# Kernel optimization log

Measured on AMD Instinct MI355X. Metric: run time of the kernel, lower is better.

The kernel has to match this reference:

```python
import jax, jax.numpy as jnp
import numpy as np

MARGIN = 0.3
N = 8192
D = 256
NUM_CLASSES = 64


def setup_inputs() -> dict:
    key = jax.random.key(0)
    k1, k2 = jax.random.split(key)
    embeddings = jax.random.normal(k1, (N, D), dtype=jnp.float32)
    labels = jax.random.randint(k2, (N,), 0, NUM_CLASSES, dtype=jnp.int64)
    return {"embeddings": embeddings, "labels": labels}


def _pairwise_euclidean(x):
    # torch.cdist(x, x, p=2): sqrt of squared distances, safe at 0
    sq = jnp.sum(x * x, axis=-1)                       # [N]
    d2 = sq[:, None] + sq[None, :] - 2.0 * (x @ x.T)   # [N, N]
    d2 = jnp.maximum(d2, 0.0)
    pos = d2 > 0
    return jnp.where(pos, jnp.sqrt(jnp.where(pos, d2, 1.0)), 0.0)


def reference(embeddings, labels):
    d = _pairwise_euclidean(embeddings)                # [N, N]
    same = labels[:, None] == labels[None, :]          # [N, N] pos_mask (incl. self)
    neg = ~same                                        # neg_mask
    pos_nz = same & (d > 0.0)                          # pos_dist[pos_dist > 0]

    hardest_pos = jnp.max(jnp.where(pos_nz, d, -jnp.inf), axis=1)  # [N]
    hardest_neg = jnp.min(jnp.where(neg, d, jnp.inf), axis=1)      # [N]

    # valid anchors: >1 positives (incl. self), >=1 negative, and a nonzero pos dist
    valid = (jnp.sum(same, axis=1) > 1) & jnp.any(neg, axis=1) & jnp.any(pos_nz, axis=1)

    per_anchor = jnp.where(valid,
                           jax.nn.relu(hardest_pos - hardest_neg + MARGIN),
                           0.0)
    count = jnp.sum(valid.astype(jnp.float32))
    return jnp.where(count > 0,
                     jnp.sum(per_anchor) / jnp.maximum(count, 1.0),
                     0.0)
```

## Files before the change

### kernel.cpp

```cpp
#include <hip/hip_runtime.h>


#define N_PTS 8192
#define DIM   256
#define MARGIN 0.3f

typedef __attribute__((ext_vector_type(8))) short bf16x8;
typedef __attribute__((ext_vector_type(4))) float f32x4;

__device__ __forceinline__ unsigned short f2bf(float f) {
    unsigned u = __float_as_uint(f);
    u += 0x7FFFu + ((u >> 16) & 1u);
    return (unsigned short)(u >> 16);
}

__global__ void prep_kernel(const float* __restrict__ X,
                            unsigned short* __restrict__ Xb,
                            float* __restrict__ sq) {
    int t = blockIdx.x * 256 + threadIdx.x;
    {
        int row = t >> 6, lane = t & 63;
        float4 v = reinterpret_cast<const float4*>(X)[t];
        float p = v.x * v.x + v.y * v.y + v.z * v.z + v.w * v.w;
        #pragma unroll
        for (int m = 1; m < 64; m <<= 1) p += __shfl_xor(p, m, 64);
        if (lane == 0) sq[row] = p;
    }
    {
        int i    = t & 1023;
        int Rg   = t >> 10;
        int half = i & 1;
        int lsub = (i >> 1) & 15;
        int lgrp = (i >> 5) & 3;
        int kk   = (i >> 7) & 7;
        int row  = Rg * 16 + lsub;
        int sidx = row * 64 + kk * 8 + lgrp * 2 + half;
        float4 v = reinterpret_cast<const float4*>(X)[sidx];
        ushort4 b4;
        b4.x = f2bf(v.x); b4.y = f2bf(v.y); b4.z = f2bf(v.z); b4.w = f2bf(v.w);
        reinterpret_cast<ushort4*>(Xb)[t] = b4;
    }
}

__launch_bounds__(512, 2)
__global__ void mine_kernel(const unsigned short* __restrict__ Xb,
                            const float* __restrict__ sq,
                            const int* __restrict__ labels,
                            float* __restrict__ vp,
                            float* __restrict__ vn) {
    int bid = blockIdx.x;
    int panel = bid >> 2;
    int q     = bid & 3;
    int tid = threadIdx.x;
    int w = tid >> 6, l = tid & 63;
    int wr = w >> 2, wc = w & 3;
    int lsub = l & 15, lgrp = l >> 4;

    const float INF = __int_as_float(0x7f800000);

    const unsigned short* abase = Xb + (size_t)(panel * 8 + wr * 4) * 4096 + l * 8;
    bf16x8 a[4][8];
    #pragma unroll
    for (int m = 0; m < 4; ++m)
        #pragma unroll
        for (int kk = 0; kk < 8; ++kk)
            a[m][kk] = *reinterpret_cast<const bf16x8*>(abase + m * 4096 + kk * 512);

    int rowbase = panel * 128 + wr * 64;
    int lrj[4][4];
    #pragma unroll
    for (int m = 0; m < 4; ++m)
        #pragma unroll
        for (int j = 0; j < 4; ++j)
            lrj[m][j] = labels[rowbase + m * 16 + lgrp * 4 + j];

    float vpr[4][4], vnr[4][4];
    #pragma unroll
    for (int m = 0; m < 4; ++m)
        #pragma unroll
        for (int j = 0; j < 4; ++j) { vpr[m][j] = -INF; vnr[m][j] = INF; }

    int colwave = q * 2048 + wc * 512;
    const unsigned short* bbase = Xb + (size_t)(colwave >> 4) * 4096 + l * 8;

    for (int cs = 0; cs < 16; ++cs) {
        int colbase = colwave + cs * 32;
        int lc0 = labels[colbase + lsub];
        int lc1 = labels[colbase + 16 + lsub];
        float sc0 = sq[colbase + lsub];
        float sc1 = sq[colbase + 16 + lsub];

        f32x4 acc[4][2];
        #pragma unroll
        for (int m = 0; m < 4; ++m) {
            acc[m][0] = (f32x4){0.f, 0.f, 0.f, 0.f};
            acc[m][1] = (f32x4){0.f, 0.f, 0.f, 0.f};
        }

        const unsigned short* bb = bbase + (size_t)cs * 8192;
        #pragma unroll
        for (int kp = 0; kp < 4; ++kp) {
            bf16x8 b00 = *reinterpret_cast<const bf16x8*>(bb + kp * 1024);
            bf16x8 b01 = *reinterpret_cast<const bf16x8*>(bb + 4096 + kp * 1024);
            bf16x8 b10 = *reinterpret_cast<const bf16x8*>(bb + kp * 1024 + 512);
            bf16x8 b11 = *reinterpret_cast<const bf16x8*>(bb + 4096 + kp * 1024 + 512);
            #pragma unroll
            for (int m = 0; m < 4; ++m) {
                acc[m][0] = __builtin_amdgcn_mfma_f32_16x16x32_bf16(
                    a[m][2 * kp], b00, acc[m][0], 0, 0, 0);
                acc[m][1] = __builtin_amdgcn_mfma_f32_16x16x32_bf16(
                    a[m][2 * kp], b01, acc[m][1], 0, 0, 0);
            }
            #pragma unroll
            for (int m = 0; m < 4; ++m) {
                acc[m][0] = __builtin_amdgcn_mfma_f32_16x16x32_bf16(
                    a[m][2 * kp + 1], b10, acc[m][0], 0, 0, 0);
                acc[m][1] = __builtin_amdgcn_mfma_f32_16x16x32_bf16(
                    a[m][2 * kp + 1], b11, acc[m][1], 0, 0, 0);
            }
        }

        #pragma unroll
        for (int m = 0; m < 4; ++m)
            #pragma unroll
            for (int j = 0; j < 4; ++j) {
                int lr = lrj[m][j];
                float v0 = fmaf(-2.f, acc[m][0][j], sc0);
                float v1 = fmaf(-2.f, acc[m][1][j], sc1);
                bool s0 = (lr == lc0), s1 = (lr == lc1);
                vpr[m][j] = fmaxf(vpr[m][j], s0 ? v0 : -INF);
                vpr[m][j] = fmaxf(vpr[m][j], s1 ? v1 : -INF);
                vnr[m][j] = fminf(vnr[m][j], s0 ? INF : v0);
                vnr[m][j] = fminf(vnr[m][j], s1 ? INF : v1);
            }
    }

    int slot = q * 4 + wc;
    #pragma unroll
    for (int m = 0; m < 4; ++m)
        #pragma unroll
        for (int j = 0; j < 4; ++j) {
            float p = vpr[m][j], n = vnr[m][j];
            #pragma unroll
            for (int s = 1; s < 16; s <<= 1) {
                p = fmaxf(p, __shfl_xor(p, s, 64));
                n = fminf(n, __shfl_xor(n, s, 64));
            }
            if (lsub == 0) {
                int row = rowbase + m * 16 + lgrp * 4 + j;
                vp[slot * N_PTS + row] = p;
                vn[slot * N_PTS + row] = n;
            }
        }
}

__global__ void finalizeA_kernel(const float* __restrict__ vp,
                                 const float* __restrict__ vn,
                                 const float* __restrict__ sq,
                                 const int* __restrict__ labels,
                                 float* __restrict__ bsum,
                                 float* __restrict__ bcnt) {
    __shared__ int hist[64];
    __shared__ float ss[4], cc[4];
    int tid = threadIdx.x;
    if (tid < 64) hist[tid] = 0;
    __syncthreads();
    for (int i = tid; i < N_PTS; i += 256) atomicAdd(&hist[labels[i]], 1);
    __syncthreads();

    const float INF = __int_as_float(0x7f800000);
    int r = blockIdx.x * 256 + tid;
    float mp = -INF, mn = INF;
    #pragma unroll
    for (int s = 0; s < 16; ++s) {
        mp = fmaxf(mp, vp[s * N_PTS + r]);
        mn = fminf(mn, vn[s * N_PTS + r]);
    }
    float sr = sq[r];
    float hp2 = sr + mp;
    float hn2 = fmaxf(sr + mn, 0.f);
    int h = hist[labels[r]];
    bool valid = (h > 1) && (h < N_PTS) && (hp2 > 0.f);
    float contrib = valid ? fmaxf(sqrtf(hp2) - sqrtf(hn2) + MARGIN, 0.f) : 0.f;
    float cnt = valid ? 1.f : 0.f;

    #pragma unroll
    for (int m = 1; m < 64; m <<= 1) {
        contrib += __shfl_xor(contrib, m, 64);
        cnt     += __shfl_xor(cnt, m, 64);
    }
    int wv = tid >> 6, lv = tid & 63;
    if (lv == 0) { ss[wv] = contrib; cc[wv] = cnt; }
    __syncthreads();
    if (tid == 0) {
        bsum[blockIdx.x] = ss[0] + ss[1] + ss[2] + ss[3];
        bcnt[blockIdx.x] = cc[0] + cc[1] + cc[2] + cc[3];
    }
}

__global__ void finalizeB_kernel(const float* __restrict__ bsum,
                                 const float* __restrict__ bcnt,
                                 float* __restrict__ out) {
    int l = threadIdx.x;
    float s = (l < 32) ? bsum[l] : 0.f;
    float c = (l < 32) ? bcnt[l] : 0.f;
    #pragma unroll
    for (int m = 1; m < 64; m <<= 1) {
        s += __shfl_xor(s, m, 64);
        c += __shfl_xor(c, m, 64);
    }
    if (l == 0) out[0] = (c > 0.f) ? (s / c) : 0.f;
}

extern "C" void kernel_launch(void* const* d_in, const int* in_sizes, int n_in,
                              void* d_out, int out_size, void* d_ws, size_t ws_size,
                              hipStream_t stream) {
    const float* X      = (const float*)d_in[0];
    const int*   labels = (const int*)d_in[1];
    float*       out    = (float*)d_out;

    char* ws = (char*)d_ws;
    unsigned short* Xb = (unsigned short*)ws;
    float* sq   = (float*)(ws + 4194304);
    float* vp   = (float*)(ws + 4194304 + 32768);
    float* vn   = (float*)(ws + 4194304 + 32768 + 524288);
    float* bsum = (float*)(ws + 4194304 + 32768 + 1048576);
    float* bcnt = (float*)(ws + 4194304 + 32768 + 1048576 + 128);

    prep_kernel<<<2048, 256, 0, stream>>>(X, Xb, sq);
    mine_kernel<<<256, 512, 0, stream>>>(Xb, sq, labels, vp, vn);
    finalizeA_kernel<<<32, 256, 0, stream>>>(vp, vn, sq, labels, bsum, bcnt);
    finalizeB_kernel<<<1, 64, 0, stream>>>(bsum, bcnt, out);
}
```

Baseline: 112.9 us.

## Restructure mining kernel with LDS-staged row bands, register-resident columns, fused finalize

The mining kernel now holds a 64-column B tile in registers per wave and streams 512-row bands through double-buffered, XOR-swizzled LDS using global_load_lds, with a swizzled block order. It writes per-column partial max/min, relying on the symmetry of the distance matrix. The prep kernel drops the fragment-layout repack in favour of plain row-major bf16, and the two finalize kernels merge into one that uses atomics and a last-block counter. The aim is better reuse and fewer launches, at the cost of LDS traffic, barriers, and atomic ordering risk.

```diff
diff --git a/kernel.cpp b/kernel.cpp
--- a/kernel.cpp
+++ b/kernel.cpp
@@ -14,32 +14,23 @@
     return (unsigned short)(u >> 16);
 }
 
-__global__ void prep_kernel(const float* __restrict__ X,
-                            unsigned short* __restrict__ Xb,
-                            float* __restrict__ sq) {
+__global__ __launch_bounds__(256)
+void prep_kernel(const float* __restrict__ X,
+                 unsigned short* __restrict__ Xb,
+                 float* __restrict__ sq,
+                 float* __restrict__ gsum) {
     int t = blockIdx.x * 256 + threadIdx.x;
-    {
-        int row = t >> 6, lane = t & 63;
-        float4 v = reinterpret_cast<const float4*>(X)[t];
-        float p = v.x * v.x + v.y * v.y + v.z * v.z + v.w * v.w;
-        #pragma unroll
-        for (int m = 1; m < 64; m <<= 1) p += __shfl_xor(p, m, 64);
-        if (lane == 0) sq[row] = p;
-    }
-    {
-        int i    = t & 1023;
-        int Rg   = t >> 10;
-        int half = i & 1;
-        int lsub = (i >> 1) & 15;
-        int lgrp = (i >> 5) & 3;
-        int kk   = (i >> 7) & 7;
-        int row  = Rg * 16 + lsub;
-        int sidx = row * 64 + kk * 8 + lgrp * 2 + half;
-        float4 v = reinterpret_cast<const float4*>(X)[sidx];
-        ushort4 b4;
-        b4.x = f2bf(v.x); b4.y = f2bf(v.y); b4.z = f2bf(v.z); b4.w = f2bf(v.w);
-        reinterpret_cast<ushort4*>(Xb)[t] = b4;
-    }
+    int row = t >> 6, lane = t & 63;
+    float4 v = reinterpret_cast<const float4*>(X)[t];
+    ushort4 b4;
+    b4.x = f2bf(v.x); b4.y = f2bf(v.y); b4.z = f2bf(v.z); b4.w = f2bf(v.w);
+    reinterpret_cast<ushort4*>(Xb)[t] = b4;
+    float p = v.x * v.x + v.y * v.y + v.z * v.z + v.w * v.w;
+    #pragma unroll
+    for (int m = 1; m < 64; m <<= 1) p += __shfl_xor(p, m, 64);
+    if (lane == 0) sq[row] = p;
+    if (blockIdx.x == 0 && threadIdx.x < 3)
+        gsum[threadIdx.x] = 0.f;
 }
 
 __launch_bounds__(512, 2)
@@ -48,118 +39,138 @@
                             const int* __restrict__ labels,
                             float* __restrict__ vp,
                             float* __restrict__ vn) {
+    __shared__ unsigned short buf[2][64 * 256];
+
     int bid = blockIdx.x;
-    int panel = bid >> 2;
-    int q     = bid & 3;
+    int swz = (bid & 7) * 32 + (bid >> 3);
+    int cg = swz >> 4;
+    int rb = swz & 15;
+
     int tid = threadIdx.x;
     int w = tid >> 6, l = tid & 63;
-    int wr = w >> 2, wc = w & 3;
     int lsub = l & 15, lgrp = l >> 4;
+    int C0 = cg * 512 + w * 64;
 
     const float INF = __int_as_float(0x7f800000);
 
-    const unsigned short* abase = Xb + (size_t)(panel * 8 + wr * 4) * 4096 + l * 8;
-    bf16x8 a[4][8];
-    #pragma unroll
-    for (int m = 0; m < 4; ++m)
-        #pragma unroll
-        for (int kk = 0; kk < 8; ++kk)
-            a[m][kk] = *reinterpret_cast<const bf16x8*>(abase + m * 4096 + kk * 512);
-
-    int rowbase = panel * 128 + wr * 64;
-    int lrj[4][4];
-    #pragma unroll
-    for (int m = 0; m < 4; ++m)
-        #pragma unroll
-        for (int j = 0; j < 4; ++j)
-            lrj[m][j] = labels[rowbase + m * 16 + lgrp * 4 + j];
-
-    float vpr[4][4], vnr[4][4];
-    #pragma unroll
-    for (int m = 0; m < 4; ++m)
-        #pragma unroll
-        for (int j = 0; j < 4; ++j) { vpr[m][j] = -INF; vnr[m][j] = INF; }
-
-    int colwave = q * 2048 + wc * 512;
-    const unsigned short* bbase = Xb + (size_t)(colwave >> 4) * 4096 + l * 8;
-
-    for (int cs = 0; cs < 16; ++cs) {
-        int colbase = colwave + cs * 32;
-        int lc0 = labels[colbase + lsub];
-        int lc1 = labels[colbase + 16 + lsub];
-        float sc0 = sq[colbase + lsub];
-        float sc1 = sq[colbase + 16 + lsub];
-
-        f32x4 acc[4][2];
-        #pragma unroll
-        for (int m = 0; m < 4; ++m) {
-            acc[m][0] = (f32x4){0.f, 0.f, 0.f, 0.f};
-            acc[m][1] = (f32x4){0.f, 0.f, 0.f, 0.f};
-        }
-
-        const unsigned short* bb = bbase + (size_t)cs * 8192;
-        #pragma unroll
-        for (int kp = 0; kp < 4; ++kp) {
-            bf16x8 b00 = *reinterpret_cast<const bf16x8*>(bb + kp * 1024);
-            bf16x8 b01 = *reinterpret_cast<const bf16x8*>(bb + 4096 + kp * 1024);
-            bf16x8 b10 = *reinterpret_cast<const bf16x8*>(bb + kp * 1024 + 512);
-            bf16x8 b11 = *reinterpret_cast<const bf16x8*>(bb + 4096 + kp * 1024 + 512);
+    bf16x8 b[4][8];
+    {
+        const unsigned short* pb = Xb + (size_t)(C0 + lsub) * DIM + lgrp * 8;
+        #pragma unroll
+        for (int n = 0; n < 4; ++n)
+            #pragma unroll
+            for (int kk = 0; kk < 8; ++kk)
+                b[n][kk] = *reinterpret_cast<const bf16x8*>(
+                    pb + (size_t)n * 16 * DIM + kk * 32);
+    }
+    int lc4[4];
+    #pragma unroll
+    for (int n = 0; n < 4; ++n) lc4[n] = labels[C0 + n * 16 + lsub];
+
+    float hpc[4], hnc[4];
+    #pragma unroll
+    for (int n = 0; n < 4; ++n) { hpc[n] = -INF; hnc[n] = INF; }
+
+    int band = rb * 512;
+    int xorv = lsub & 7;
+
+    {
+        const unsigned short* src = Xb + (size_t)band * DIM;
+        #pragma unroll
+        for (int i = 0; i < 4; ++i) {
+            int p = i * 512 + tid;
+            int row = p >> 5, slot = p & 31;
+            int kc = slot ^ (row & 7);
+            __builtin_amdgcn_global_load_lds(
+                (const __attribute__((address_space(1))) void*)(src + row * DIM + kc * 8),
+                (__attribute__((address_space(3))) void*)(&buf[0][p * 8]),
+                16, 0, 0);
+        }
+    }
+    __syncthreads();
+
+    int cur = 0;
+    for (int c = 0; c < 8; ++c) {
+        if (c < 7) {
+            const unsigned short* src = Xb + (size_t)(band + (c + 1) * 64) * DIM;
+            #pragma unroll
+            for (int i = 0; i < 4; ++i) {
+                int p = i * 512 + tid;
+                int row = p >> 5, slot = p & 31;
+                int kc = slot ^ (row & 7);
+                __builtin_amdgcn_global_load_lds(
+                    (const __attribute__((address_space(1))) void*)(src + row * DIM + kc * 8),
+                    (__attribute__((address_space(3))) void*)(&buf[cur ^ 1][p * 8]),
+                    16, 0, 0);
+            }
+        }
+
+        const unsigned short* bc = buf[cur];
+        f32x4 acc[4][4];
+        #pragma unroll
+        for (int m = 0; m < 4; ++m)
+            #pragma unroll
+            for (int n = 0; n < 4; ++n) acc[m][n] = (f32x4){0.f, 0.f, 0.f, 0.f};
+
+        #pragma unroll
+        for (int kk = 0; kk < 8; ++kk) {
+            bf16x8 a[4];
             #pragma unroll
             for (int m = 0; m < 4; ++m) {
-                acc[m][0] = __builtin_amdgcn_mfma_f32_16x16x32_bf16(
-                    a[m][2 * kp], b00, acc[m][0], 0, 0, 0);
-                acc[m][1] = __builtin_amdgcn_mfma_f32_16x16x32_bf16(
-                    a[m][2 * kp], b01, acc[m][1], 0, 0, 0);
+                int rowA = m * 16 + lsub;
+                int slot = (kk * 4 + lgrp) ^ xorv;
+                a[m] = *reinterpret_cast<const bf16x8*>(&bc[rowA * 256 + slot * 8]);
             }
             #pragma unroll
-            for (int m = 0; m < 4; ++m) {
-                acc[m][0] = __builtin_amdgcn_mfma_f32_16x16x32_bf16(
-                    a[m][2 * kp + 1], b10, acc[m][0], 0, 0, 0);
-                acc[m][1] = __builtin_amdgcn_mfma_f32_16x16x32_bf16(
-                    a[m][2 * kp + 1], b11, acc[m][1], 0, 0, 0);
+            for (int m = 0; m < 4; ++m)
+                #pragma unroll
+                for (int n = 0; n < 4; ++n)
+                    acc[m][n] = __builtin_amdgcn_mfma_f32_16x16x32_bf16(
+                        a[m], b[n][kk], acc[m][n], 0, 0, 0);
+        }
+
+        int rowg = band + c * 64 + lgrp * 4;
+        #pragma unroll
+        for (int m = 0; m < 4; ++m)
+            #pragma unroll
+            for (int j = 0; j < 4; ++j) {
+                int gr = rowg + m * 16 + j;
+                int lr = labels[gr];
+                float sr = sq[gr];
+                #pragma unroll
+                for (int n = 0; n < 4; ++n) {
+                    float v = fmaf(-2.f, acc[m][n][j], sr);
+                    bool same = (lr == lc4[n]);
+                    hpc[n] = same ? fmaxf(hpc[n], v) : hpc[n];
+                    hnc[n] = same ? hnc[n] : fminf(hnc[n], v);
+                }
             }
-        }
-
-        #pragma unroll
-        for (int m = 0; m < 4; ++m)
-            #pragma unroll
-            for (int j = 0; j < 4; ++j) {
-                int lr = lrj[m][j];
-                float v0 = fmaf(-2.f, acc[m][0][j], sc0);
-                float v1 = fmaf(-2.f, acc[m][1][j], sc1);
-                bool s0 = (lr == lc0), s1 = (lr == lc1);
-                vpr[m][j] = fmaxf(vpr[m][j], s0 ? v0 : -INF);
-                vpr[m][j] = fmaxf(vpr[m][j], s1 ? v1 : -INF);
-                vnr[m][j] = fminf(vnr[m][j], s0 ? INF : v0);
-                vnr[m][j] = fminf(vnr[m][j], s1 ? INF : v1);
-            }
-    }
-
-    int slot = q * 4 + wc;
-    #pragma unroll
-    for (int m = 0; m < 4; ++m)
-        #pragma unroll
-        for (int j = 0; j < 4; ++j) {
-            float p = vpr[m][j], n = vnr[m][j];
-            #pragma unroll
-            for (int s = 1; s < 16; s <<= 1) {
-                p = fmaxf(p, __shfl_xor(p, s, 64));
-                n = fminf(n, __shfl_xor(n, s, 64));
-            }
-            if (lsub == 0) {
-                int row = rowbase + m * 16 + lgrp * 4 + j;
-                vp[slot * N_PTS + row] = p;
-                vn[slot * N_PTS + row] = n;
-            }
-        }
-}
-
-__global__ void finalizeA_kernel(const float* __restrict__ vp,
-                                 const float* __restrict__ vn,
-                                 const float* __restrict__ sq,
-                                 const int* __restrict__ labels,
-                                 float* __restrict__ bsum,
-                                 float* __restrict__ bcnt) {
+
+        if (c < 7) __syncthreads();
+        cur ^= 1;
+    }
+
+    #pragma unroll
+    for (int n = 0; n < 4; ++n) {
+        float p = hpc[n], q = hnc[n];
+        p = fmaxf(p, __shfl_xor(p, 16, 64));
+        q = fminf(q, __shfl_xor(q, 16, 64));
+        p = fmaxf(p, __shfl_xor(p, 32, 64));
+        q = fminf(q, __shfl_xor(q, 32, 64));
+        if (l < 16) {
+            int col = C0 + n * 16 + l;
+            vp[rb * N_PTS + col] = p;
+            vn[rb * N_PTS + col] = q;
+        }
+    }
+}
+
+__global__ void finalize_kernel(const float* __restrict__ vp,
+                                const float* __restrict__ vn,
+                                const float* __restrict__ sq,
+                                const int* __restrict__ labels,
+                                float* __restrict__ gsum,
+                                float* __restrict__ out) {
     __shared__ int hist[64];
     __shared__ float ss[4], cc[4];
     int tid = threadIdx.x;
@@ -169,18 +180,18 @@
     __syncthreads();
 
     const float INF = __int_as_float(0x7f800000);
-    int r = blockIdx.x * 256 + tid;
+    int c = blockIdx.x * 256 + tid;
     float mp = -INF, mn = INF;
     #pragma unroll
     for (int s = 0; s < 16; ++s) {
-        mp = fmaxf(mp, vp[s * N_PTS + r]);
-        mn = fminf(mn, vn[s * N_PTS + r]);
-    }
-    float sr = sq[r];
-    float hp2 = sr + mp;
-    float hn2 = fmaxf(sr + mn, 0.f);
-    int h = hist[labels[r]];
-    bool valid = (h > 1) && (h < N_PTS) && (hp2 > 0.f);
+        mp = fmaxf(mp, vp[s * N_PTS + c]);
+        mn = fminf(mn, vn[s * N_PTS + c]);
+    }
+    float sc = sq[c];
+    float hp2 = sc + mp;
+    float hn2 = fmaxf(sc + mn, 0.f);
+    int h = hist[labels[c]];
+    bool valid = (h > 1) && (hp2 > 0.f);
     float contrib = valid ? fmaxf(sqrtf(hp2) - sqrtf(hn2) + MARGIN, 0.f) : 0.f;
     float cnt = valid ? 1.f : 0.f;
 
@@ -193,23 +204,16 @@
     if (lv == 0) { ss[wv] = contrib; cc[wv] = cnt; }
     __syncthreads();
     if (tid == 0) {
-        bsum[blockIdx.x] = ss[0] + ss[1] + ss[2] + ss[3];
-        bcnt[blockIdx.x] = cc[0] + cc[1] + cc[2] + cc[3];
-    }
-}
-
-__global__ void finalizeB_kernel(const float* __restrict__ bsum,
-                                 const float* __restrict__ bcnt,
-                                 float* __restrict__ out) {
-    int l = threadIdx.x;
-    float s = (l < 32) ? bsum[l] : 0.f;
-    float c = (l < 32) ? bcnt[l] : 0.f;
-    #pragma unroll
-    for (int m = 1; m < 64; m <<= 1) {
-        s += __shfl_xor(s, m, 64);
-        c += __shfl_xor(c, m, 64);
-    }
-    if (l == 0) out[0] = (c > 0.f) ? (s / c) : 0.f;
+        atomicAdd(&gsum[0], ss[0] + ss[1] + ss[2] + ss[3]);
+        atomicAdd(&gsum[1], cc[0] + cc[1] + cc[2] + cc[3]);
+        __threadfence();
+        unsigned old = atomicAdd(reinterpret_cast<unsigned*>(&gsum[2]), 1u);
+        if (old == 31u) {
+            float S = atomicAdd(&gsum[0], 0.f);
+            float C = atomicAdd(&gsum[1], 0.f);
+            out[0] = (C > 0.f) ? (S / C) : 0.f;
+        }
+    }
 }
 
 extern "C" void kernel_launch(void* const* d_in, const int* in_sizes, int n_in,
@@ -224,11 +228,9 @@
     float* sq   = (float*)(ws + 4194304);
     float* vp   = (float*)(ws + 4194304 + 32768);
     float* vn   = (float*)(ws + 4194304 + 32768 + 524288);
-    float* bsum = (float*)(ws + 4194304 + 32768 + 1048576);
-    float* bcnt = (float*)(ws + 4194304 + 32768 + 1048576 + 128);
-
-    prep_kernel<<<2048, 256, 0, stream>>>(X, Xb, sq);
+    float* gsum = (float*)(ws + 4194304 + 32768 + 1048576);
+
+    prep_kernel<<<2048, 256, 0, stream>>>(X, Xb, sq, gsum);
     mine_kernel<<<256, 512, 0, stream>>>(Xb, sq, labels, vp, vn);
-    finalizeA_kernel<<<32, 256, 0, stream>>>(vp, vn, sq, labels, bsum, bcnt);
-    finalizeB_kernel<<<1, 64, 0, stream>>>(bsum, bcnt, out);
-}
+    finalize_kernel<<<32, 256, 0, stream>>>(vp, vn, sq, labels, gsum, out);
+}
```

Measured after the change: 123.3 us. 1.09x slower.
